# Kernel tuning notes

Measured on AMD Instinct MI355X. Metric: run time of the kernel, lower is better.

## Reference

```python
import jax, jax.numpy as jnp
import numpy as np

NEG_SLOPE = 0.1
LN_EPS = 1e-5


def setup_inputs() -> dict:
    key = jax.random.key(0)
    ks = jax.random.split(key, 8)
    B, S, IN, OUT, H = 16, 1024, 512, 512, 8
    DH = OUT // H
    x = jax.random.normal(ks[0], (B, S, IN), dtype=jnp.float32)
    scale = 1.0 / np.sqrt(IN)
    # per-head projection weights, stored as [H, in, dh] so y = x @ W
    wq = jax.random.uniform(ks[1], (H, IN, DH), minval=-scale, maxval=scale, dtype=jnp.float32)
    wk = jax.random.uniform(ks[2], (H, IN, DH), minval=-scale, maxval=scale, dtype=jnp.float32)
    wv = jax.random.uniform(ks[3], (H, IN, DH), minval=-scale, maxval=scale, dtype=jnp.float32)
    scale_o = 1.0 / np.sqrt(OUT)
    w_out = jax.random.uniform(ks[4], (OUT, OUT), minval=-scale_o, maxval=scale_o, dtype=jnp.float32)
    b_out = jax.random.uniform(ks[5], (OUT,), minval=-scale_o, maxval=scale_o, dtype=jnp.float32)
    ln_gamma = jnp.ones((OUT,), dtype=jnp.float32)
    ln_beta = jnp.zeros((OUT,), dtype=jnp.float32)
    return {"x": x, "wq": wq, "wk": wk, "wv": wv, "w_out": w_out,
            "b_out": b_out, "ln_gamma": ln_gamma, "ln_beta": ln_beta}


def reference(x, wq, wk, wv, w_out, b_out, ln_gamma, ln_beta):
    B, S, _ = x.shape
    H, _, DH = wq.shape
    # per-head projections, vectorized over heads: [H, B, S, DH]
    q = jnp.einsum('bsf,hfd->hbsd', x, wq)
    k = jnp.einsum('bsf,hfd->hbsd', x, wk)
    v = jnp.einsum('bsf,hfd->hbsd', x, wv)
    # attention scores [H, B, S, S]
    att = jnp.einsum('hbsd,hbtd->hbst', q, k) / jnp.sqrt(jnp.float32(DH))
    # FAITHFUL to source: softmax over dim=0 of the per-head [B,S,S] tensor,
    # i.e. the BATCH axis (axis=1 in our [H,B,S,S] layout)
    att = jax.nn.softmax(att, axis=1)
    out = jnp.einsum('hbst,hbtd->hbsd', att, v)
    # concat heads -> [B, S, H*DH]
    heads_cat = jnp.transpose(out, (1, 2, 0, 3)).reshape(B, S, H * DH)
    y = heads_cat @ w_out + b_out
    # LayerNorm over last dim
    mu = jnp.mean(y, axis=-1, keepdims=True)
    var = jnp.var(y, axis=-1, keepdims=True)
    y = (y - mu) * jax.lax.rsqrt(var + LN_EPS) * ln_gamma + ln_beta
    # LeakyReLU(0.1)
    return jnp.where(y >= 0, y, NEG_SLOPE * y)
```

## Files before the change

kernel.cpp:

```cpp
#include <hip/hip_runtime.h>

typedef unsigned short u16;
typedef unsigned int uint;
typedef __attribute__((ext_vector_type(8))) short bf16x8;
typedef __attribute__((ext_vector_type(4))) float f32x4;

#define NBATCH 16
#define SDIM   1024
#define INDIM  512
#define OUTDIM 512
#define HEADS  8
#define DHEAD  64
#define MROWS  (NBATCH * SDIM)
#define KDIM   512

__device__ __forceinline__ u16 f2bf(float f) {
  union { float f; uint u; } v; v.f = f;
  uint u = v.u;
  return (u16)((u + 0x7FFFu + ((u >> 16) & 1u)) >> 16);
}

__device__ __forceinline__ uint pkbf(float a, float b) {
  return (uint)f2bf(a) | ((uint)f2bf(b) << 16);
}

__device__ __forceinline__ float bf2f(u16 v) {
  union { uint u; float f; } c; c.u = (uint)v << 16;
  return c.f;
}

__device__ __forceinline__ void gload16(const void* g, void* l) {
  __builtin_amdgcn_global_load_lds(
      (const __attribute__((address_space(1))) uint*)g,
      (__attribute__((address_space(3))) uint*)l, 16, 0, 0);
}

__global__ __launch_bounds__(256) void prep_kernel(
    const float* __restrict__ x, const float* __restrict__ wq,
    const float* __restrict__ wk, const float* __restrict__ wv,
    const float* __restrict__ w_out,
    u16* __restrict__ xb, u16* __restrict__ W1T, u16* __restrict__ W2T) {
  int gid = blockIdx.x * blockDim.x + threadIdx.x;
  int stride = gridDim.x * blockDim.x;
  const int NX4 = MROWS * INDIM / 4;
  for (int i = gid; i < NX4; i += stride) {
    float4 v = ((const float4*)x)[i];
    ((ushort4*)xb)[i] = make_ushort4(f2bf(v.x), f2bf(v.y), f2bf(v.z), f2bf(v.w));
  }
  for (int i = gid; i < 3 * OUTDIM * INDIM; i += stride) {
    int n = i >> 9, f = i & 511;
    int proj = n >> 9, hd = n & 511, h = hd >> 6, d = hd & 63;
    const float* src = (proj == 0) ? wq : (proj == 1) ? wk : wv;
    float val = src[(h * INDIM + f) * DHEAD + d];
    if (proj == 0) val *= 0.125f;
    W1T[i] = f2bf(val);
  }
  for (int i = gid; i < OUTDIM * INDIM; i += stride) {
    int n = i >> 9, f = i & 511;
    W2T[i] = f2bf(w_out[f * OUTDIM + n]);
  }
}

template <int EPI>
__global__ __launch_bounds__(256) void gemm128(
    const u16* __restrict__ A, const u16* __restrict__ Bt,
    u16* __restrict__ Qb, u16* __restrict__ Kb, u16* __restrict__ VTb,
    float* __restrict__ Y) {
  __shared__ u16 As[128 * 32];
  __shared__ u16 Bs[128 * 32];
  const int tid = threadIdx.x;
  const int w = tid >> 6, lane = tid & 63;
  const int quad = lane >> 4, ln = lane & 15;
  const int wm = w >> 1, wn = w & 1;
  const int m0 = blockIdx.y * 128, n0 = blockIdx.x * 128;

  f32x4 zero4 = {0.f, 0.f, 0.f, 0.f};
  f32x4 acc[4][4];
  for (int i = 0; i < 4; i++)
    for (int j = 0; j < 4; j++) acc[i][j] = zero4;

  const char* Ag = (const char*)(A + (size_t)m0 * KDIM);
  const char* Bg = (const char*)(Bt + (size_t)n0 * KDIM);
  const int r0 = w * 16 + (lane >> 2);
  const int cb = (lane & 3) * 16;

  for (int kk = 0; kk < KDIM; kk += 32) {
    __syncthreads();
    gload16(Ag + (size_t)r0 * (KDIM * 2) + kk * 2 + cb, (char*)As + w * 1024);
    gload16(Ag + (size_t)(r0 + 64) * (KDIM * 2) + kk * 2 + cb, (char*)As + 4096 + w * 1024);
    gload16(Bg + (size_t)r0 * (KDIM * 2) + kk * 2 + cb, (char*)Bs + w * 1024);
    gload16(Bg + (size_t)(r0 + 64) * (KDIM * 2) + kk * 2 + cb, (char*)Bs + 4096 + w * 1024);
    __syncthreads();
    bf16x8 af[4], bfr[4];
    for (int mt = 0; mt < 4; mt++)
      af[mt] = *(const bf16x8*)&As[(wm * 64 + mt * 16 + ln) * 32 + quad * 8];
    for (int nt = 0; nt < 4; nt++)
      bfr[nt] = *(const bf16x8*)&Bs[(wn * 64 + nt * 16 + ln) * 32 + quad * 8];
    for (int mt = 0; mt < 4; mt++)
      for (int nt = 0; nt < 4; nt++)
        acc[mt][nt] = __builtin_amdgcn_mfma_f32_16x16x32_bf16(af[mt], bfr[nt], acc[mt][nt], 0, 0, 0);
  }

  for (int mt = 0; mt < 4; mt++) {
    int mbase = m0 + wm * 64 + mt * 16 + quad * 4;
    int b = mbase >> 10, sbase = mbase & 1023;
    for (int nt = 0; nt < 4; nt++) {
      f32x4 c = acc[mt][nt];
      int col = n0 + wn * 64 + nt * 16 + ln;
      if (EPI == 0) {
        int proj = n0 >> 9;
        int hd = col & 511, h = hd >> 6, d = hd & 63;
        if (proj == 2) {
          *(ushort4*)&VTb[((size_t)(h * 16 + b) * 64 + d) * 1024 + sbase] =
              make_ushort4(f2bf(c[0]), f2bf(c[1]), f2bf(c[2]), f2bf(c[3]));
        } else {
          u16* dst = (proj == 0) ? Qb : Kb;
          size_t base = ((size_t)(h * 16 + b) * 1024) * 64 + d;
          dst[base + (size_t)(sbase + 0) * 64] = f2bf(c[0]);
          dst[base + (size_t)(sbase + 1) * 64] = f2bf(c[1]);
          dst[base + (size_t)(sbase + 2) * 64] = f2bf(c[2]);
          dst[base + (size_t)(sbase + 3) * 64] = f2bf(c[3]);
        }
      } else {
        Y[(size_t)(mbase + 0) * OUTDIM + col] = c[0];
        Y[(size_t)(mbase + 1) * OUTDIM + col] = c[1];
        Y[(size_t)(mbase + 2) * OUTDIM + col] = c[2];
        Y[(size_t)(mbase + 3) * OUTDIM + col] = c[3];
      }
    }
  }
}

__global__ __launch_bounds__(512, 4) void attnA_kernel(
    const u16* __restrict__ Qb, const u16* __restrict__ Kb,
    u16* __restrict__ LinvX) {
  __shared__ u16 Qt[2 * 64 * 64];
  __shared__ u16 Kt[2 * 128 * 64];
  const int tid = threadIdx.x;
  const int w = tid >> 6, lane = tid & 63;
  const int quad = lane >> 4, ln = lane & 15;
  const int ws = w & 3, wt = w >> 2;
  const int h = blockIdx.x & 7;
  const int s0 = ((blockIdx.x >> 3) & 15) * 64;
  const int tblk = blockIdx.x >> 7;
  const int t0 = tblk * 128;
  const int srow = tid >> 3, sseg = tid & 7;

  const u16* Qh = Qb + (size_t)h * 16 * 65536;
  const u16* Kh = Kb + (size_t)h * 16 * 65536;

  f32x4 zero4 = {0.f, 0.f, 0.f, 0.f};
  f32x4 Lacc[4];
  for (int i = 0; i < 4; i++) Lacc[i] = zero4;

  {
    gload16(Qh + (size_t)(s0 + srow) * 64 + sseg * 8, (char*)Qt + w * 1024);
    const u16* Kg = Kh + (size_t)(t0 + srow) * 64 + sseg * 8;
    gload16(Kg, (char*)Kt + w * 1024);
    gload16(Kg + 64 * 64, (char*)Kt + 8192 + w * 1024);
  }

  for (int b = 0; b < 16; b++) {
    const int cur = b & 1;
    __syncthreads();
    if (b < 15) {
      const u16* Qg = Qh + (size_t)(b + 1) * 65536 + (size_t)(s0 + srow) * 64 + sseg * 8;
      const u16* Kg = Kh + (size_t)(b + 1) * 65536 + (size_t)(t0 + srow) * 64 + sseg * 8;
      gload16(Qg, (char*)Qt + (cur ^ 1) * 8192 + w * 1024);
      gload16(Kg, (char*)Kt + (cur ^ 1) * 16384 + w * 1024);
      gload16(Kg + 64 * 64, (char*)Kt + (cur ^ 1) * 16384 + 8192 + w * 1024);
    }
    const u16* Qr = &Qt[cur * 4096 + (ws * 16 + ln) * 64];
    bf16x8 q0 = *(const bf16x8*)&Qr[quad * 8];
    bf16x8 q1 = *(const bf16x8*)&Qr[32 + quad * 8];
    for (int tsub = 0; tsub < 4; tsub++) {
      const u16* Kr = &Kt[cur * 8192 + (wt * 64 + tsub * 16 + ln) * 64];
      f32x4 cc = zero4;
      cc = __builtin_amdgcn_mfma_f32_16x16x32_bf16(*(const bf16x8*)&Kr[quad * 8], q0, cc, 0, 0, 0);
      cc = __builtin_amdgcn_mfma_f32_16x16x32_bf16(*(const bf16x8*)&Kr[32 + quad * 8], q1, cc, 0, 0, 0);
      f32x4 L = Lacc[tsub];
      L[0] += __expf(cc[0]); L[1] += __expf(cc[1]);
      L[2] += __expf(cc[2]); L[3] += __expf(cc[3]);
      Lacc[tsub] = L;
    }
  }

  const int sg = s0 + ws * 16 + ln;
  for (int tsub = 0; tsub < 4; tsub++) {
    const int tc = tblk * 8 + wt * 4 + tsub;
    f32x4 L = Lacc[tsub];
    uint2 pk = make_uint2(
        pkbf(__builtin_amdgcn_rcpf(L[0]), __builtin_amdgcn_rcpf(L[1])),
        pkbf(__builtin_amdgcn_rcpf(L[2]), __builtin_amdgcn_rcpf(L[3])));
    *(uint2*)&LinvX[(((size_t)(h * 64 + tc)) * 1024 + sg) * 16 + quad * 4] = pk;
  }
}

__global__ __launch_bounds__(256, 4) void attnB_kernel(
    const u16* __restrict__ Qb, const u16* __restrict__ Kb,
    const u16* __restrict__ VTb, const u16* __restrict__ LinvX,
    u16* __restrict__ hc) {
  __shared__ u16 Ks[2 * 32 * 64];
  __shared__ u16 Vs[2 * 64 * 32];
  __shared__ u16 Pp[4 * 2 * 16 * 40];
  const int tid = threadIdx.x;
  const int w = tid >> 6, lane = tid & 63;
  const int quad = lane >> 4, ln = lane & 15;
  const int h = blockIdx.x & 7, b = (blockIdx.x >> 3) & 15, sblk = blockIdx.x >> 7;
  const int ss0 = sblk * 128 + w * 32;
  const int krow = tid >> 3, kseg = tid & 7;
  const int vrow = tid >> 2, vseg = tid & 3;

  const u16* Kbase = Kb + (size_t)(h * 16 + b) * 65536;
  const u16* Vbase = VTb + (size_t)(h * 16 + b) * 65536;
  const u16* LinvH = LinvX + (size_t)h * 64 * 1024 * 16;

  f32x4 zero4 = {0.f, 0.f, 0.f, 0.f};
  bf16x8 qf[2][2];
  for (int a = 0; a < 2; a++) {
    const u16* Qp = Qb + ((size_t)(h * 16 + b) * 1024 + ss0 + a * 16 + ln) * 64;
    qf[a][0] = *(const bf16x8*)&Qp[quad * 8];
    qf[a][1] = *(const bf16x8*)&Qp[32 + quad * 8];
  }
  f32x4 o[2][4];
  for (int a = 0; a < 2; a++)
    for (int df = 0; df < 4; df++) o[a][df] = zero4;

  gload16(Kbase + (size_t)krow * 64 + kseg * 8, (char*)Ks + w * 1024);
  gload16(Vbase + (size_t)vrow * 1024 + vseg * 8, (char*)Vs + w * 1024);

  for (int it = 0; it < 32; ++it) {
    const int cur = it & 1;
    const int t0 = it * 32;
    __syncthreads();
    if (it < 31) {
      gload16(Kbase + (size_t)(t0 + 32 + krow) * 64 + kseg * 8,
              (char*)Ks + (cur ^ 1) * 4096 + w * 1024);
      gload16(Vbase + (size_t)vrow * 1024 + t0 + 32 + vseg * 8,
              (char*)Vs + (cur ^ 1) * 4096 + w * 1024);
    }
    bf16x8 kf[2][2], vf[4];
    for (int tsub = 0; tsub < 2; tsub++) {
      const u16* Kr = &Ks[cur * 2048 + (tsub * 16 + ln) * 64];
      kf[tsub][0] = *(const bf16x8*)&Kr[quad * 8];
      kf[tsub][1] = *(const bf16x8*)&Kr[32 + quad * 8];
    }
    for (int df = 0; df < 4; df++)
      vf[df] = *(const bf16x8*)&Vs[cur * 2048 + (df * 16 + ln) * 32 + quad * 8];

    for (int a = 0; a < 2; a++) {
      for (int tsub = 0; tsub < 2; tsub++) {
        const int tc = it * 2 + tsub;
        ushort4 lin = *(const ushort4*)&LinvH[
            (((size_t)tc) * 1024 + ss0 + a * 16 + ln) * 16 + quad * 4];
        f32x4 cc = zero4;
        cc = __builtin_amdgcn_mfma_f32_16x16x32_bf16(kf[tsub][0], qf[a][0], cc, 0, 0, 0);
        cc = __builtin_amdgcn_mfma_f32_16x16x32_bf16(kf[tsub][1], qf[a][1], cc, 0, 0, 0);
        f32x4 p;
        p[0] = __expf(cc[0]) * bf2f(lin.x);
        p[1] = __expf(cc[1]) * bf2f(lin.y);
        p[2] = __expf(cc[2]) * bf2f(lin.z);
        p[3] = __expf(cc[3]) * bf2f(lin.w);
        uint2 pk = make_uint2(pkbf(p[0], p[1]), pkbf(p[2], p[3]));
        *(uint2*)&Pp[(w * 2 + a) * 640 + ln * 40 + tsub * 16 + quad * 4] = pk;
      }
      bf16x8 pa = *(const bf16x8*)&Pp[(w * 2 + a) * 640 + ln * 40 + quad * 8];
      for (int df = 0; df < 4; df++)
        o[a][df] = __builtin_amdgcn_mfma_f32_16x16x32_bf16(pa, vf[df], o[a][df], 0, 0, 0);
    }
  }

  for (int a = 0; a < 2; a++) {
    for (int df = 0; df < 4; df++) {
      f32x4 c = o[a][df];
      for (int r = 0; r < 4; r++) {
        int sg = ss0 + a * 16 + quad * 4 + r;
        hc[((size_t)(b * 1024 + sg)) * 512 + h * 64 + df * 16 + ln] = f2bf(c[r]);
      }
    }
  }
}

__global__ __launch_bounds__(256) void ln_kernel(
    const float* __restrict__ Y, const float* __restrict__ b_out,
    const float* __restrict__ gamma, const float* __restrict__ beta,
    float* __restrict__ out) {
  const int w = threadIdx.x >> 6, lane = threadIdx.x & 63;
  const int row = blockIdx.x * 4 + w;
  const float4* yr = (const float4*)(Y + (size_t)row * 512);
  float4 v0 = yr[lane], v1 = yr[64 + lane];
  float4 b0 = ((const float4*)b_out)[lane], b1 = ((const float4*)b_out)[64 + lane];
  v0.x += b0.x; v0.y += b0.y; v0.z += b0.z; v0.w += b0.w;
  v1.x += b1.x; v1.y += b1.y; v1.z += b1.z; v1.w += b1.w;
  float s  = v0.x + v0.y + v0.z + v0.w + v1.x + v1.y + v1.z + v1.w;
  float s2 = v0.x * v0.x + v0.y * v0.y + v0.z * v0.z + v0.w * v0.w +
             v1.x * v1.x + v1.y * v1.y + v1.z * v1.z + v1.w * v1.w;
  for (int off = 32; off; off >>= 1) {
    s += __shfl_xor(s, off);
    s2 += __shfl_xor(s2, off);
  }
  float mean = s * (1.0f / 512.0f);
  float var = s2 * (1.0f / 512.0f) - mean * mean;
  float rs = rsqrtf(var + 1e-5f);
  float4 g0 = ((const float4*)gamma)[lane], g1 = ((const float4*)gamma)[64 + lane];
  float4 e0 = ((const float4*)beta)[lane], e1 = ((const float4*)beta)[64 + lane];
  float4 o0, o1;
  o0.x = (v0.x - mean) * rs * g0.x + e0.x;  o0.y = (v0.y - mean) * rs * g0.y + e0.y;
  o0.z = (v0.z - mean) * rs * g0.z + e0.z;  o0.w = (v0.w - mean) * rs * g0.w + e0.w;
  o1.x = (v1.x - mean) * rs * g1.x + e1.x;  o1.y = (v1.y - mean) * rs * g1.y + e1.y;
  o1.z = (v1.z - mean) * rs * g1.z + e1.z;  o1.w = (v1.w - mean) * rs * g1.w + e1.w;
  o0.x = o0.x >= 0.f ? o0.x : 0.1f * o0.x;  o0.y = o0.y >= 0.f ? o0.y : 0.1f * o0.y;
  o0.z = o0.z >= 0.f ? o0.z : 0.1f * o0.z;  o0.w = o0.w >= 0.f ? o0.w : 0.1f * o0.w;
  o1.x = o1.x >= 0.f ? o1.x : 0.1f * o1.x;  o1.y = o1.y >= 0.f ? o1.y : 0.1f * o1.y;
  o1.z = o1.z >= 0.f ? o1.z : 0.1f * o1.z;  o1.w = o1.w >= 0.f ? o1.w : 0.1f * o1.w;
  ((float4*)out)[(size_t)row * 128 + lane] = o0;
  ((float4*)out)[(size_t)row * 128 + 64 + lane] = o1;
}

extern "C" void kernel_launch(void* const* d_in, const int* in_sizes, int n_in,
                              void* d_out, int out_size, void* d_ws, size_t ws_size,
                              hipStream_t stream) {
  const float* x      = (const float*)d_in[0];
  const float* wq     = (const float*)d_in[1];
  const float* wk     = (const float*)d_in[2];
  const float* wv     = (const float*)d_in[3];
  const float* w_out  = (const float*)d_in[4];
  const float* b_out  = (const float*)d_in[5];
  const float* gamma  = (const float*)d_in[6];
  const float* beta   = (const float*)d_in[7];
  float* out = (float*)d_out;

  char* ws = (char*)d_ws;
  size_t off = 0;
  u16* xb  = (u16*)(ws + off); off += (size_t)MROWS * INDIM * 2;
  u16* W1T = (u16*)(ws + off); off += (size_t)3 * OUTDIM * INDIM * 2;
  u16* W2T = (u16*)(ws + off); off += (size_t)OUTDIM * INDIM * 2;
  u16* Qb  = (u16*)(ws + off); off += (size_t)HEADS * NBATCH * SDIM * DHEAD * 2;
  u16* Kb  = (u16*)(ws + off); off += (size_t)HEADS * NBATCH * SDIM * DHEAD * 2;
  u16* VTb = (u16*)(ws + off); off += (size_t)HEADS * NBATCH * SDIM * DHEAD * 2;
  u16* hc  = (u16*)(ws + off); off += (size_t)MROWS * OUTDIM * 2;
  float* Yv = (float*)(ws + off);
  u16* LinvX = (u16*)Yv;

  prep_kernel<<<2048, 256, 0, stream>>>(x, wq, wk, wv, w_out, xb, W1T, W2T);
  gemm128<0><<<dim3(12, 128), 256, 0, stream>>>(xb, W1T, Qb, Kb, VTb, nullptr);
  attnA_kernel<<<1024, 512, 0, stream>>>(Qb, Kb, LinvX);
  attnB_kernel<<<1024, 256, 0, stream>>>(Qb, Kb, VTb, LinvX, hc);
  gemm128<1><<<dim3(4, 128), 256, 0, stream>>>(hc, W2T, nullptr, nullptr, nullptr, Yv);
  ln_kernel<<<4096, 256, 0, stream>>>(Yv, b_out, gamma, beta, out);
}
```

Baseline: 266.1 us.

## Swizzle attention LDS tiles, fold log2e into Q scale, use exp2 and fast bf16 pack

Applies an XOR swizzle to the global-to-LDS loads of Q, K and V tiles in both attention kernels, with matching swizzled fragment reads, to cut LDS bank conflicts. Folds log2(e) into the Q weight scaling so the softmax exponentials become raw exp2 instructions with no extra multiply. Replaces round-to-nearest-even bf16 packing of probabilities with a cheaper add-and-permute round-half-up pack, which slightly changes rounding.

After: 439.5 us. +65.1%, slower.

```diff
diff --git a/kernel.cpp b/kernel.cpp
--- a/kernel.cpp
+++ b/kernel.cpp
@@ -13,6 +13,7 @@
 #define DHEAD  64
 #define MROWS  (NBATCH * SDIM)
 #define KDIM   512
+#define QSCALE (0.125f * 1.44269504088896340736f)
 
 __device__ __forceinline__ u16 f2bf(float f) {
   union { float f; uint u; } v; v.f = f;
@@ -22,6 +23,11 @@
 
 __device__ __forceinline__ uint pkbf(float a, float b) {
   return (uint)f2bf(a) | ((uint)f2bf(b) << 16);
+}
+
+__device__ __forceinline__ uint pkbf_fast(float a, float b) {
+  union { float f; uint u; } ua, ub; ua.f = a; ub.f = b;
+  return __builtin_amdgcn_perm(ub.u + 0x8000u, ua.u + 0x8000u, 0x07060302);
 }
 
 __device__ __forceinline__ float bf2f(u16 v) {
@@ -52,7 +58,7 @@
     int proj = n >> 9, hd = n & 511, h = hd >> 6, d = hd & 63;
     const float* src = (proj == 0) ? wq : (proj == 1) ? wk : wv;
     float val = src[(h * INDIM + f) * DHEAD + d];
-    if (proj == 0) val *= 0.125f;
+    if (proj == 0) val *= QSCALE;
     W1T[i] = f2bf(val);
   }
   for (int i = gid; i < OUTDIM * INDIM; i += stride) {
@@ -144,7 +150,8 @@
   const int s0 = ((blockIdx.x >> 3) & 15) * 64;
   const int tblk = blockIdx.x >> 7;
   const int t0 = tblk * 128;
-  const int srow = tid >> 3, sseg = tid & 7;
+  const int srow = tid >> 3;
+  const int ssw = ((tid & 7) ^ (srow & 7)) * 8;
 
   const u16* Qh = Qb + (size_t)h * 16 * 65536;
   const u16* Kh = Kb + (size_t)h * 16 * 65536;
@@ -154,33 +161,35 @@
   for (int i = 0; i < 4; i++) Lacc[i] = zero4;
 
   {
-    gload16(Qh + (size_t)(s0 + srow) * 64 + sseg * 8, (char*)Qt + w * 1024);
-    const u16* Kg = Kh + (size_t)(t0 + srow) * 64 + sseg * 8;
+    gload16(Qh + (size_t)(s0 + srow) * 64 + ssw, (char*)Qt + w * 1024);
+    const u16* Kg = Kh + (size_t)(t0 + srow) * 64 + ssw;
     gload16(Kg, (char*)Kt + w * 1024);
     gload16(Kg + 64 * 64, (char*)Kt + 8192 + w * 1024);
   }
+
+  const int fsw = (quad ^ (ln & 7)) * 8;
 
   for (int b = 0; b < 16; b++) {
     const int cur = b & 1;
     __syncthreads();
     if (b < 15) {
-      const u16* Qg = Qh + (size_t)(b + 1) * 65536 + (size_t)(s0 + srow) * 64 + sseg * 8;
-      const u16* Kg = Kh + (size_t)(b + 1) * 65536 + (size_t)(t0 + srow) * 64 + sseg * 8;
+      const u16* Qg = Qh + (size_t)(b + 1) * 65536 + (size_t)(s0 + srow) * 64 + ssw;
+      const u16* Kg = Kh + (size_t)(b + 1) * 65536 + (size_t)(t0 + srow) * 64 + ssw;
       gload16(Qg, (char*)Qt + (cur ^ 1) * 8192 + w * 1024);
       gload16(Kg, (char*)Kt + (cur ^ 1) * 16384 + w * 1024);
       gload16(Kg + 64 * 64, (char*)Kt + (cur ^ 1) * 16384 + 8192 + w * 1024);
     }
     const u16* Qr = &Qt[cur * 4096 + (ws * 16 + ln) * 64];
-    bf16x8 q0 = *(const bf16x8*)&Qr[quad * 8];
-    bf16x8 q1 = *(const bf16x8*)&Qr[32 + quad * 8];
+    bf16x8 q0 = *(const bf16x8*)&Qr[fsw];
+    bf16x8 q1 = *(const bf16x8*)&Qr[fsw ^ 32];
     for (int tsub = 0; tsub < 4; tsub++) {
       const u16* Kr = &Kt[cur * 8192 + (wt * 64 + tsub * 16 + ln) * 64];
       f32x4 cc = zero4;
-      cc = __builtin_amdgcn_mfma_f32_16x16x32_bf16(*(const bf16x8*)&Kr[quad * 8], q0, cc, 0, 0, 0);
-      cc = __builtin_amdgcn_mfma_f32_16x16x32_bf16(*(const bf16x8*)&Kr[32 + quad * 8], q1, cc, 0, 0, 0);
+      cc = __builtin_amdgcn_mfma_f32_16x16x32_bf16(*(const bf16x8*)&Kr[fsw], q0, cc, 0, 0, 0);
+      cc = __builtin_amdgcn_mfma_f32_16x16x32_bf16(*(const bf16x8*)&Kr[fsw ^ 32], q1, cc, 0, 0, 0);
       f32x4 L = Lacc[tsub];
-      L[0] += __expf(cc[0]); L[1] += __expf(cc[1]);
-      L[2] += __expf(cc[2]); L[3] += __expf(cc[3]);
+      L[0] += __builtin_amdgcn_exp2f(cc[0]); L[1] += __builtin_amdgcn_exp2f(cc[1]);
+      L[2] += __builtin_amdgcn_exp2f(cc[2]); L[3] += __builtin_amdgcn_exp2f(cc[3]);
       Lacc[tsub] = L;
     }
   }
@@ -208,8 +217,10 @@
   const int quad = lane >> 4, ln = lane & 15;
   const int h = blockIdx.x & 7, b = (blockIdx.x >> 3) & 15, sblk = blockIdx.x >> 7;
   const int ss0 = sblk * 128 + w * 32;
-  const int krow = tid >> 3, kseg = tid & 7;
-  const int vrow = tid >> 2, vseg = tid & 3;
+  const int krow = tid >> 3;
+  const int ksw = ((tid & 7) ^ (krow & 7)) * 8;
+  const int vrow = tid >> 2;
+  const int vsw = ((tid & 3) ^ ((tid >> 3) & 3)) * 8;
 
   const u16* Kbase = Kb + (size_t)(h * 16 + b) * 65536;
   const u16* Vbase = VTb + (size_t)(h * 16 + b) * 65536;
@@ -226,27 +237,30 @@
   for (int a = 0; a < 2; a++)
     for (int df = 0; df < 4; df++) o[a][df] = zero4;
 
-  gload16(Kbase + (size_t)krow * 64 + kseg * 8, (char*)Ks + w * 1024);
-  gload16(Vbase + (size_t)vrow * 1024 + vseg * 8, (char*)Vs + w * 1024);
+  gload16(Kbase + (size_t)krow * 64 + ksw, (char*)Ks + w * 1024);
+  gload16(Vbase + (size_t)vrow * 1024 + vsw, (char*)Vs + w * 1024);
+
+  const int fsw = (quad ^ (ln & 7)) * 8;
+  const int vfsw = (quad ^ ((ln >> 1) & 3)) * 8;
 
   for (int it = 0; it < 32; ++it) {
     const int cur = it & 1;
     const int t0 = it * 32;
     __syncthreads();
     if (it < 31) {
-      gload16(Kbase + (size_t)(t0 + 32 + krow) * 64 + kseg * 8,
+      gload16(Kbase + (size_t)(t0 + 32 + krow) * 64 + ksw,
               (char*)Ks + (cur ^ 1) * 4096 + w * 1024);
-      gload16(Vbase + (size_t)vrow * 1024 + t0 + 32 + vseg * 8,
+      gload16(Vbase + (size_t)vrow * 1024 + t0 + 32 + vsw,
               (char*)Vs + (cur ^ 1) * 4096 + w * 1024);
     }
     bf16x8 kf[2][2], vf[4];
     for (int tsub = 0; tsub < 2; tsub++) {
       const u16* Kr = &Ks[cur * 2048 + (tsub * 16 + ln) * 64];
-      kf[tsub][0] = *(const bf16x8*)&Kr[quad * 8];
-      kf[tsub][1] = *(const bf16x8*)&Kr[32 + quad * 8];
+      kf[tsub][0] = *(const bf16x8*)&Kr[fsw];
+      kf[tsub][1] = *(const bf16x8*)&Kr[fsw ^ 32];
     }
     for (int df = 0; df < 4; df++)
-      vf[df] = *(const bf16x8*)&Vs[cur * 2048 + (df * 16 + ln) * 32 + quad * 8];
+      vf[df] = *(const bf16x8*)&Vs[cur * 2048 + (df * 16 + ln) * 32 + vfsw];
 
     for (int a = 0; a < 2; a++) {
       for (int tsub = 0; tsub < 2; tsub++) {
@@ -256,12 +270,11 @@
         f32x4 cc = zero4;
         cc = __builtin_amdgcn_mfma_f32_16x16x32_bf16(kf[tsub][0], qf[a][0], cc, 0, 0, 0);
         cc = __builtin_amdgcn_mfma_f32_16x16x32_bf16(kf[tsub][1], qf[a][1], cc, 0, 0, 0);
-        f32x4 p;
-        p[0] = __expf(cc[0]) * bf2f(lin.x);
-        p[1] = __expf(cc[1]) * bf2f(lin.y);
-        p[2] = __expf(cc[2]) * bf2f(lin.z);
-        p[3] = __expf(cc[3]) * bf2f(lin.w);
-        uint2 pk = make_uint2(pkbf(p[0], p[1]), pkbf(p[2], p[3]));
+        float p0 = __builtin_amdgcn_exp2f(cc[0]) * bf2f(lin.x);
+        float p1 = __builtin_amdgcn_exp2f(cc[1]) * bf2f(lin.y);
+        float p2 = __builtin_amdgcn_exp2f(cc[2]) * bf2f(lin.z);
+        float p3 = __builtin_amdgcn_exp2f(cc[3]) * bf2f(lin.w);
+        uint2 pk = make_uint2(pkbf_fast(p0, p1), pkbf_fast(p2, p3));
         *(uint2*)&Pp[(w * 2 + a) * 640 + ln * 40 + tsub * 16 + quad * 4] = pk;
       }
       bf16x8 pa = *(const bf16x8*)&Pp[(w * 2 + a) * 640 + ln * 40 + quad * 8];
```
